# Optimization experiments

Measured on AMD Instinct MI355X. Metric: run time of the kernel, lower is better.

Reference implementation:

```python
import jax, jax.numpy as jnp
import numpy as np

NX, NQ, NU = 2048, 2048, 16
EPS = 0.01
STD = 0.5


def setup_inputs() -> dict:
    key = jax.random.key(0)
    ks = jax.random.split(key, 8)
    return {
        "t": 0,
        "x": jax.random.normal(ks[0], (NX,), dtype=jnp.float32),
        "u": jax.random.normal(ks[1], (NU,), dtype=jnp.float32),
        "X": jax.random.normal(ks[2], (NX + NQ, NX + NQ), dtype=jnp.float32) * STD,
        "U": jax.random.normal(ks[3], (NX, NQ), dtype=jnp.float32) * STD,
        "Y1": jax.random.normal(ks[4], (NX, NX), dtype=jnp.float32) * STD,
        "XP": jax.random.normal(ks[5], (NX, NX), dtype=jnp.float32) * STD,
        "B2": jax.random.normal(ks[6], (NX, NU), dtype=jnp.float32) * STD,
        "D12": jax.random.normal(ks[7], (NQ, NU), dtype=jnp.float32) * STD,
    }


def _constrained_mats(X, U, Y1, XP):
    nx = XP.shape[0]
    nq = U.shape[1]
    # P = XP XP^T + eps I ;  H = X X^T + eps I   (F.linear(A,B)=A@B.T)
    P = XP @ XP.T + EPS * jnp.eye(nx, dtype=XP.dtype)
    H = X @ X.T + EPS * jnp.eye(nx + nq, dtype=X.dtype)
    H11 = H[:nx, :nx]
    H12 = H[:nx, nx:]
    H22 = H[nx:, nx:]
    Y = -0.5 * (H11 + Y1 - Y1.T)
    Pinv = jnp.linalg.inv(P)
    A = Pinv @ Y                        # F.linear(inv(P), Y.T) = inv(P) @ Y
    lam = 0.5 * jnp.diagonal(H22)       # diagonal of Lambda
    D11 = -jnp.tril(H22, -1) / lam[:, None]   # strictly lower triangular
    C1 = U.T / lam[:, None]             # inv(Lambda) @ U.T
    B1 = Pinv @ (-H12 - U)
    return A, B1, C1, D11


def _solve_w(D11, c):
    nq = c.shape[0]

    def step(w, inp):
        i, d_row, ci = inp
        wi = jax.nn.relu(ci + jnp.dot(d_row, w))
        return w.at[i].set(wi), None

    w0 = jnp.zeros(nq, dtype=c.dtype)
    w, _ = jax.lax.scan(step, w0, (jnp.arange(nq), D11, c))
    return w


def reference(t, x, u, X, U, Y1, XP, B2, D12):
    A, B1, C1, D11 = _constrained_mats(X, U, Y1, XP)
    c = C1 @ x + D12 @ u                # precomputed affine part (bv = 0, bias=False)
    w = _solve_w(D11, c)
    x_dot = A @ x + B1 @ w + B2 @ u     # bx = 0
    return x_dot
```

## Files before the change

kernel.cpp:

```cpp
#include <hip/hip_runtime.h>
#include <math.h>

#define NQ2 2048
#define NT  4096
#define NUU 16
#define FEPS 0.01f
#define NB  64
#define NBLK 32
#define NSB 128
#define NSP 132
#define NSBLK 16
#define GCH 16

typedef __attribute__((ext_vector_type(8))) short short8;
typedef __attribute__((ext_vector_type(4))) float floatx4;

__device__ __forceinline__ float readlane_f(float v, int lane) {
  return __int_as_float(__builtin_amdgcn_readlane(__float_as_int(v), lane));
}
__device__ __forceinline__ unsigned short f2bf(float x) {
  unsigned u = __float_as_uint(x);
  unsigned r = u + 0x7FFFu + ((u >> 16) & 1u);
  return (unsigned short)(r >> 16);
}
__device__ __forceinline__ float bf2f(unsigned short h) {
  return __uint_as_float(((unsigned)h) << 16);
}

__device__ __forceinline__ float wave_reduce(float v) {
#pragma unroll
  for (int off = 32; off > 0; off >>= 1) v += __shfl_down(v, off, 64);
  return v;
}
__device__ __forceinline__ float block_reduce_256(float v) {
  __shared__ float sm[4];
  v = wave_reduce(v);
  if ((threadIdx.x & 63) == 0) sm[threadIdx.x >> 6] = v;
  __syncthreads();
  return (threadIdx.x == 0) ? (sm[0] + sm[1] + sm[2] + sm[3]) : 0.0f;
}

__global__ __launch_bounds__(256) void lam_kernel(const float* __restrict__ X,
                                                  float* __restrict__ invlam) {
  int row = blockIdx.x;
  const float* xr = X + (size_t)(NQ2 + row) * NT;
  float s = 0.f;
  for (int k = threadIdx.x * 4; k < NT; k += 1024) {
    float4 v = *(const float4*)(xr + k);
    s += v.x * v.x + v.y * v.y + v.z * v.z + v.w * v.w;
  }
  float tot = block_reduce_256(s);
  if (threadIdx.x == 0) invlam[row] = 1.0f / (0.5f * (tot + FEPS));
}

__global__ __launch_bounds__(256) void tgemv_part_kernel(const float* __restrict__ A,
                                                         const float* __restrict__ v,
                                                         float* __restrict__ part) {
  int col = blockIdx.x * 256 + threadIdx.x;
  int ch = blockIdx.y;
  int i0 = ch * (NQ2 / GCH), i1 = i0 + NQ2 / GCH;
  float s = 0.f;
#pragma unroll 4
  for (int i = i0; i < i1; i++) s = fmaf(A[(size_t)i * NQ2 + col], v[i], s);
  part[(size_t)ch * NQ2 + col] = s;
}

template <int FM>
__global__ __launch_bounds__(256) void finish_kernel(const float* __restrict__ part,
                                                     const float* __restrict__ invlam,
                                                     const float* __restrict__ D12,
                                                     const float* __restrict__ u,
                                                     float* __restrict__ dst) {
  int col = blockIdx.x * 256 + threadIdx.x;
  float s = 0.f;
#pragma unroll
  for (int ch = 0; ch < GCH; ch++) s += part[(size_t)ch * NQ2 + col];
  if (FM == 0) {
    float d = 0.f;
#pragma unroll
    for (int j = 0; j < NUU; j++) d += D12[(size_t)col * NUU + j] * u[j];
    dst[col] = s * invlam[col] + d;
  } else if (FM == 1) {
    dst[col] += 0.5f * s;
  } else {
    dst[col] = s;
  }
}

__device__ void syrk512_body(const float* __restrict__ A, int lda, int K,
                             float* __restrict__ C, float eps, int L, int tid) {
  __shared__ __align__(16) short Ah[4096], Al[4096], Bh[4096], Bl[4096];

  int bi = (int)((sqrtf(8.0f * (float)L + 1.0f) - 1.0f) * 0.5f);
  while ((bi + 1) * (bi + 2) / 2 <= L) bi++;
  while (bi * (bi + 1) / 2 > L) bi--;
  int bj = L - bi * (bi + 1) / 2;
  int row0 = bi * 128, col0 = bj * 128;

  int l = tid & 63;
  int w = tid >> 6;
  int wr = w >> 1, wc = w & 1;

  int g = tid;
  int ar = (g >> 6) * 16 + (g & 15), ak = ((g >> 4) & 3) * 8;
  const float* pa = A + (size_t)(row0 + ar) * lda + ak;
  const float* pb = A + (size_t)(col0 + ar) * lda + ak;

  floatx4 acc[4][4];
#pragma unroll
  for (int m = 0; m < 4; m++)
#pragma unroll
    for (int n = 0; n < 4; n++) acc[m][n] = (floatx4){0.f, 0.f, 0.f, 0.f};

  float xa[8], xb[8];
  {
    float4 t0 = *(const float4*)(pa), t1 = *(const float4*)(pa + 4);
    xa[0]=t0.x; xa[1]=t0.y; xa[2]=t0.z; xa[3]=t0.w; xa[4]=t1.x; xa[5]=t1.y; xa[6]=t1.z; xa[7]=t1.w;
    t0 = *(const float4*)(pb); t1 = *(const float4*)(pb + 4);
    xb[0]=t0.x; xb[1]=t0.y; xb[2]=t0.z; xb[3]=t0.w; xb[4]=t1.x; xb[5]=t1.y; xb[6]=t1.z; xb[7]=t1.w;
  }

  for (int k0 = 0; k0 < K; k0 += 32) {
    __syncthreads();
    {
      short8 h, lo;
#pragma unroll
      for (int j = 0; j < 8; j++) { unsigned short hb = f2bf(xa[j]); h[j] = (short)hb; lo[j] = (short)f2bf(xa[j] - bf2f(hb)); }
      *(short8*)&Ah[g * 8] = h; *(short8*)&Al[g * 8] = lo;
#pragma unroll
      for (int j = 0; j < 8; j++) { unsigned short hb = f2bf(xb[j]); h[j] = (short)hb; lo[j] = (short)f2bf(xb[j] - bf2f(hb)); }
      *(short8*)&Bh[g * 8] = h; *(short8*)&Bl[g * 8] = lo;
    }
    __syncthreads();
    if (k0 + 32 < K) {
      const float* q = pa + k0 + 32;
      float4 t0 = *(const float4*)(q), t1 = *(const float4*)(q + 4);
      xa[0]=t0.x; xa[1]=t0.y; xa[2]=t0.z; xa[3]=t0.w; xa[4]=t1.x; xa[5]=t1.y; xa[6]=t1.z; xa[7]=t1.w;
      q = pb + k0 + 32; t0 = *(const float4*)(q); t1 = *(const float4*)(q + 4);
      xb[0]=t0.x; xb[1]=t0.y; xb[2]=t0.z; xb[3]=t0.w; xb[4]=t1.x; xb[5]=t1.y; xb[6]=t1.z; xb[7]=t1.w;
    }
    if (tid < 256) {
      short8 amh[4], aml[4], bnh[4], bnl[4];
#pragma unroll
      for (int m = 0; m < 4; m++) {
        int ga = ((wr * 4 + m) * 64 + l) * 8;
        amh[m] = *(const short8*)&Ah[ga];
        aml[m] = *(const short8*)&Al[ga];
      }
#pragma unroll
      for (int n = 0; n < 4; n++) {
        int gb = ((wc * 4 + n) * 64 + l) * 8;
        bnh[n] = *(const short8*)&Bh[gb];
        bnl[n] = *(const short8*)&Bl[gb];
      }
#pragma unroll
      for (int m = 0; m < 4; m++)
#pragma unroll
        for (int n = 0; n < 4; n++) {
          acc[m][n] = __builtin_amdgcn_mfma_f32_16x16x32_bf16(amh[m], bnh[n], acc[m][n], 0, 0, 0);
          acc[m][n] = __builtin_amdgcn_mfma_f32_16x16x32_bf16(amh[m], bnl[n], acc[m][n], 0, 0, 0);
          acc[m][n] = __builtin_amdgcn_mfma_f32_16x16x32_bf16(aml[m], bnh[n], acc[m][n], 0, 0, 0);
        }
    }
  }

  if (tid < 256) {
    int lr = (l >> 4) * 4;
    int lc = l & 15;
#pragma unroll
    for (int m = 0; m < 4; m++)
#pragma unroll
      for (int n = 0; n < 4; n++)
#pragma unroll
        for (int r = 0; r < 4; r++) {
          int gi = row0 + wr * 64 + m * 16 + lr + r;
          int gj = col0 + wc * 64 + n * 16 + lc;
          float v = acc[m][n][r];
          if (gi == gj) v += eps;
          C[(size_t)gi * NQ2 + gj] = v;
        }
  }
}

__global__ __launch_bounds__(512) void syrk512_kernel(const float* __restrict__ A,
                                                      int lda, int K,
                                                      float* __restrict__ C, float eps) {
  syrk512_body(A, lda, K, C, eps, blockIdx.x, threadIdx.x);
}

__device__ void wsolve_body(const float* __restrict__ M_, const float* __restrict__ rhs,
                            const float* __restrict__ invlam, float* __restrict__ out,
                            int tid) {
  __shared__ float partial[NQ2];
  __shared__ float il[NQ2];
  __shared__ float tile[2][NB][NB + 1];
  __shared__ float vblk[NB];
  int rquad = tid >> 2;
  int l4 = tid & 3;
  for (int i = tid; i < NQ2; i += 512) {
    partial[i] = rhs[i];
    il[i] = invlam[i];
  }
  for (int e = tid; e < NB * NB; e += 512) {
    int rr = e >> 6, cc = e & 63;
    tile[0][rr][cc] = M_[(size_t)rr * NQ2 + cc];
  }
  __syncthreads();
  for (int b = 0; b < NBLK; b++) {
    int cur = b & 1;
    int b0 = b * NB;
    if (tid < 64) {
      int l = tid;
      float creg = partial[b0 + l];
      float ilreg = il[b0 + l];
      float acc = 0.f;
      float wfin = 0.f;
#pragma unroll
      for (int i = 0; i < NB; i++) {
        float cand = fmaxf(creg - acc * ilreg, 0.f);
        float wi = readlane_f(cand, i);
        acc = fmaf(tile[cur][l][i], wi, acc);
        if (l == i) wfin = wi;
      }
      vblk[l] = wfin;
      out[b0 + l] = wfin;
    } else if (b + 1 < NBLK) {
      int b1 = b0 + NB;
      for (int e = tid - 64; e < NB * NB; e += 448) {
        int rr = e >> 6, cc = e & 63;
        tile[cur ^ 1][rr][cc] = M_[(size_t)(b1 + rr) * NQ2 + b1 + cc];
      }
    }
    __syncthreads();
    float4 v0 = *(const float4*)(&vblk[l4 * 16]);
    float4 v1 = *(const float4*)(&vblk[l4 * 16 + 4]);
    float4 v2 = *(const float4*)(&vblk[l4 * 16 + 8]);
    float4 v3 = *(const float4*)(&vblk[l4 * 16 + 12]);
    for (int base = b0 + NB; base < NQ2; base += 512) {
      float accv[4] = {0.f, 0.f, 0.f, 0.f};
#pragma unroll
      for (int rr = 0; rr < 4; rr++) {
        int row = base + rr * 128 + rquad;
        if (row < NQ2) {
          const float* mr = M_ + (size_t)row * NQ2 + b0 + l4 * 16;
          float4 m0 = *(const float4*)(mr);
          float4 m1 = *(const float4*)(mr + 4);
          float4 m2 = *(const float4*)(mr + 8);
          float4 m3 = *(const float4*)(mr + 12);
          accv[rr] = m0.x * v0.x + m0.y * v0.y + m0.z * v0.z + m0.w * v0.w
                   + m1.x * v1.x + m1.y * v1.y + m1.z * v1.z + m1.w * v1.w
                   + m2.x * v2.x + m2.y * v2.y + m2.z * v2.z + m2.w * v2.w
                   + m3.x * v3.x + m3.y * v3.y + m3.z * v3.z + m3.w * v3.w;
        }
      }
#pragma unroll
      for (int rr = 0; rr < 4; rr++) {
        accv[rr] += __shfl_xor(accv[rr], 1);
        accv[rr] += __shfl_xor(accv[rr], 2);
      }
      if (l4 == 0) {
#pragma unroll
        for (int rr = 0; rr < 4; rr++) {
          int row = base + rr * 128 + rquad;
          if (row < NQ2) partial[row] -= accv[rr] * il[row];
        }
      }
    }
    __syncthreads();
  }
}

__global__ __launch_bounds__(512) void wsolve_kernel(const float* __restrict__ M_,
                                                     const float* __restrict__ rhs,
                                                     const float* __restrict__ invlam,
                                                     float* __restrict__ out) {
  wsolve_body(M_, rhs, invlam, out, threadIdx.x);
}

__global__ __launch_bounds__(512) void merged_wsolve_psyrk_kernel(
    const float* __restrict__ Mh22, const float* __restrict__ c,
    const float* __restrict__ invlam, float* __restrict__ w,
    const float* __restrict__ XP, float* __restrict__ P) {
  if (blockIdx.x == 0) {
    wsolve_body(Mh22, c, invlam, w, threadIdx.x);
  } else {
    syrk512_body(XP, NQ2, NQ2, P, FEPS, blockIdx.x - 1, threadIdx.x);
  }
}

__global__ __launch_bounds__(512) void chol_diag128_kernel(float* __restrict__ M_,
                                                           float* __restrict__ Xinvs, int k) {
  __shared__ __align__(16) float Ls[NSB][NSP];
  __shared__ __align__(16) float Xs[NSB][NSP];
  __shared__ float Tmp[32][33];
  __shared__ float dinv[NSB];
  int b0 = k * NSB;
  int tid = threadIdx.x;
  int wv = tid >> 6;
  int lane = tid & 63;

  for (int e = tid; e < NSB * NSP; e += 512) ((float*)Xs)[e] = 0.f;
  for (int e = tid; e < NSB * NSB; e += 512) {
    int rr = e >> 7, cc = e & 127;
    Ls[rr][cc] = M_[(size_t)(b0 + rr) * NQ2 + b0 + cc];
  }
  __syncthreads();

#pragma unroll 1
  for (int kb = 0; kb < 4; kb++) {
    int o = kb * 32;
    if (wv == 0) {
      int r = lane & 31;
      float a[32];
#pragma unroll
      for (int j = 0; j < 32; j++) a[j] = Ls[o + r][o + j];
#pragma unroll
      for (int j = 0; j < 32; j++) {
        float d = readlane_f(a[j], j);
        float rs = rsqrtf(fmaxf(d, 1e-20f));
        a[j] *= rs;
        if (lane == 0) dinv[o + j] = rs;
#pragma unroll
        for (int k2 = j + 1; k2 < 32; k2++) {
          float ljk = readlane_f(a[j], k2);
          a[k2] = fmaf(-a[j], ljk, a[k2]);
        }
      }
      if (lane < 32) {
#pragma unroll
        for (int j = 0; j < 32; j++) Ls[o + r][o + j] = a[j];
      }
    }
    __syncthreads();
    int nrows = 96 - o;
    if (nrows > 0) {
      if (tid < nrows) {
        int r = o + 32 + tid;
        float v[32];
#pragma unroll
        for (int j = 0; j < 32; j++) v[j] = Ls[r][o + j];
#pragma unroll
        for (int t = 0; t < 32; t++) {
          v[t] *= dinv[o + t];
#pragma unroll
          for (int j = t + 1; j < 32; j++)
            v[j] = fmaf(-v[t], Ls[o + j][o + t], v[j]);
        }
#pragma unroll
        for (int j = 0; j < 32; j++) Ls[r][o + j] = v[j];
      }
      __syncthreads();
      int tot = nrows * (nrows + 1) / 2;
      for (int e = tid; e < tot; e += 512) {
        int a = (int)((sqrtf(8.0f * (float)e + 1.0f) - 1.0f) * 0.5f);
        while ((a + 1) * (a + 2) / 2 <= e) a++;
        while (a * (a + 1) / 2 > e) a--;
        int bcol = e - a * (a + 1) / 2;
        int rr = o + 32 + a, cc = o + 32 + bcol;
        float s = 0.f;
#pragma unroll
        for (int t = 0; t < 32; t += 4) {
          float4 av = *(const float4*)&Ls[rr][o + t];
          float4 bv = *(const float4*)&Ls[cc][o + t];
          s += av.x * bv.x + av.y * bv.y + av.z * bv.z + av.w * bv.w;
        }
        Ls[rr][cc] -= s;
      }
      __syncthreads();
    }
  }

  if (wv < 4) {
    int o = wv * 32;
    int c = lane & 31;
    float x[32];
#pragma unroll
    for (int i = 0; i < 32; i++) x[i] = 0.f;
#pragma unroll
    for (int t = 0; t < 32; t++) {
      float rcpd = 1.0f / Ls[o + t][o + t];
      x[t] = (t == c) ? rcpd : x[t] * rcpd;
#pragma unroll
      for (int i = t + 1; i < 32; i++)
        x[i] = fmaf(-Ls[o + i][o + t], x[t], x[i]);
    }
    if (lane < 32) {
#pragma unroll
      for (int i = 0; i < 32; i++) Xs[o + i][o + c] = x[i];
    }
  }
  __syncthreads();

#pragma unroll 1
  for (int j = 0; j < 4; j++) {
#pragma unroll 1
    for (int i = j + 1; i < 4; i++) {
      int oi = i * 32, oj = j * 32;
      for (int e = tid; e < 32 * 32; e += 512) {
        int rr = e >> 5, cc = e & 31;
        float s = 0.f;
        for (int kk = j; kk < i; kk++) {
          int ok = kk * 32;
#pragma unroll
          for (int t = 0; t < 32; t += 4) {
            float4 a = *(const float4*)&Ls[oi + rr][ok + t];
            s += a.x * Xs[ok + t][oj + cc] + a.y * Xs[ok + t + 1][oj + cc]
               + a.z * Xs[ok + t + 2][oj + cc] + a.w * Xs[ok + t + 3][oj + cc];
          }
        }
        Tmp[rr][cc] = s;
      }
      __syncthreads();
      for (int e = tid; e < 32 * 32; e += 512) {
        int rr = e >> 5, cc = e & 31;
        float s = 0.f;
#pragma unroll
        for (int t = 0; t < 32; t += 4) {
          float4 a = *(const float4*)&Xs[oi + rr][oi + t];
          s += a.x * Tmp[t][cc] + a.y * Tmp[t + 1][cc]
             + a.z * Tmp[t + 2][cc] + a.w * Tmp[t + 3][cc];
        }
        Xs[oi + rr][oj + cc] = -s;
      }
      __syncthreads();
    }
  }

  float* Xp = Xinvs + (size_t)k * NSB * NSB;
  for (int e = tid; e < NSB * NSB; e += 512) {
    int rr = e >> 7, cc = e & 127;
    if (cc <= rr) M_[(size_t)(b0 + rr) * NQ2 + b0 + cc] = Ls[rr][cc];
    Xp[e] = Xs[rr][cc];
  }
}

__device__ void trail512_body(float* __restrict__ M_, int k, int L, int tid) {
  __shared__ float As[16][128];
  __shared__ float Bs[16][128];
  int bi = (int)((sqrtf(8.0f * (float)L + 1.0f) - 1.0f) * 0.5f);
  while ((bi + 1) * (bi + 2) / 2 <= L) bi++;
  while (bi * (bi + 1) / 2 > L) bi--;
  int bj = L - bi * (bi + 1) / 2;
  int row0 = (k + 1 + bi) * NSB, col0 = (k + 1 + bj) * NSB, kc = k * NSB;
  const float* ap = M_ + (size_t)row0 * NQ2 + kc;
  const float* bp = M_ + (size_t)col0 * NQ2 + kc;

  int tx = tid & 15, ty = (tid >> 4) & 15;
  float acc[8][8] = {{0.f}};
  for (int k0 = 0; k0 < 128; k0 += 16) {
    __syncthreads();
    for (int e = tid; e < 1024; e += 512) {
      int isB = e >> 9, idx = e & 511;
      int row = idx >> 2, q = (idx & 3) * 4;
      const float* src = isB ? bp : ap;
      float4 v = *(const float4*)(src + (size_t)row * NQ2 + k0 + q);
      if (isB) { Bs[q][row] = v.x; Bs[q + 1][row] = v.y; Bs[q + 2][row] = v.z; Bs[q + 3][row] = v.w; }
      else     { As[q][row] = v.x; As[q + 1][row] = v.y; As[q + 2][row] = v.z; As[q + 3][row] = v.w; }
    }
    __syncthreads();
    if (tid < 256) {
#pragma unroll
      for (int kk = 0; kk < 16; kk++) {
        float4 aL = *(const float4*)&As[kk][ty * 4];
        float4 aH = *(const float4*)&As[kk][64 + ty * 4];
        float4 bL = *(const float4*)&Bs[kk][tx * 4];
        float4 bH = *(const float4*)&Bs[kk][64 + tx * 4];
        float aa[8] = {aL.x, aL.y, aL.z, aL.w, aH.x, aH.y, aH.z, aH.w};
        float bb[8] = {bL.x, bL.y, bL.z, bL.w, bH.x, bH.y, bH.z, bH.w};
#pragma unroll
        for (int i = 0; i < 8; i++)
#pragma unroll
          for (int j = 0; j < 8; j++) acc[i][j] = fmaf(aa[i], bb[j], acc[i][j]);
      }
    }
  }
  if (tid < 256) {
#pragma unroll
    for (int ii = 0; ii < 8; ii++) {
      int gi = row0 + ((ii >> 2) * 64) + ty * 4 + (ii & 3);
#pragma unroll
      for (int half = 0; half < 2; half++) {
        int gj0 = col0 + half * 64 + tx * 4;
        float* cp = &M_[(size_t)gi * NQ2 + gj0];
        float4 v = *(const float4*)cp;
        v.x -= acc[ii][half * 4 + 0]; v.y -= acc[ii][half * 4 + 1];
        v.z -= acc[ii][half * 4 + 2]; v.w -= acc[ii][half * 4 + 3];
        *(float4*)cp = v;
      }
    }
  }
}

__global__ __launch_bounds__(512) void chol_trail512_kernel(float* __restrict__ M_, int k) {
  trail512_body(M_, k, blockIdx.x, threadIdx.x);
}

__global__ __launch_bounds__(256) void chol_panel128_kernel(float* __restrict__ M_,
                                                            const float* __restrict__ Xinv,
                                                            int k) {
  int kc = k * NSB;
  int rb0 = kc + NSB + blockIdx.x * 128;
  __shared__ float As[16][128];
  __shared__ float Bs[16][128];
  int tid = threadIdx.x;
  int tx = tid & 15, ty = tid >> 4;
  int sr = tid >> 1, ks = (tid & 1) * 8;

  const float* ap = M_ + (size_t)(rb0 + sr) * NQ2 + kc + ks;
  const float* bp = Xinv + sr * 128 + ks;
  float4 a0 = *(const float4*)(ap), a1 = *(const float4*)(ap + 4);
  float4 b0 = *(const float4*)(bp), b1 = *(const float4*)(bp + 4);

  float acc[8][8] = {{0.f}};
  for (int k0 = 0; k0 < 128; k0 += 16) {
    __syncthreads();
    As[ks + 0][sr] = a0.x; As[ks + 1][sr] = a0.y; As[ks + 2][sr] = a0.z; As[ks + 3][sr] = a0.w;
    As[ks + 4][sr] = a1.x; As[ks + 5][sr] = a1.y; As[ks + 6][sr] = a1.z; As[ks + 7][sr] = a1.w;
    Bs[ks + 0][sr] = b0.x; Bs[ks + 1][sr] = b0.y; Bs[ks + 2][sr] = b0.z; Bs[ks + 3][sr] = b0.w;
    Bs[ks + 4][sr] = b1.x; Bs[ks + 5][sr] = b1.y; Bs[ks + 6][sr] = b1.z; Bs[ks + 7][sr] = b1.w;
    __syncthreads();
    if (k0 + 16 < 128) {
      const float* q = ap + k0 + 16;
      a0 = *(const float4*)(q); a1 = *(const float4*)(q + 4);
      q = bp + k0 + 16;
      b0 = *(const float4*)(q); b1 = *(const float4*)(q + 4);
    }
#pragma unroll
    for (int kk = 0; kk < 16; kk++) {
      float4 aL = *(const float4*)&As[kk][ty * 4];
      float4 aH = *(const float4*)&As[kk][64 + ty * 4];
      float4 bL = *(const float4*)&Bs[kk][tx * 4];
      float4 bH = *(const float4*)&Bs[kk][64 + tx * 4];
      float aa[8] = {aL.x, aL.y, aL.z, aL.w, aH.x, aH.y, aH.z, aH.w};
      float bb[8] = {bL.x, bL.y, bL.z, bL.w, bH.x, bH.y, bH.z, bH.w};
#pragma unroll
      for (int i = 0; i < 8; i++)
#pragma unroll
        for (int j = 0; j < 8; j++) acc[i][j] = fmaf(aa[i], bb[j], acc[i][j]);
    }
  }
#pragma unroll
  for (int ii = 0; ii < 8; ii++) {
    int gi = rb0 + ((ii >> 2) * 64) + ty * 4 + (ii & 3);
#pragma unroll
    for (int half = 0; half < 2; half++) {
      int gj0 = kc + half * 64 + tx * 4;
      float4 o;
      o.x = acc[ii][half * 4 + 0]; o.y = acc[ii][half * 4 + 1];
      o.z = acc[ii][half * 4 + 2]; o.w = acc[ii][half * 4 + 3];
      *(float4*)&M_[(size_t)gi * NQ2 + gj0] = o;
    }
  }
}

__global__ __launch_bounds__(1024) void pchsolve_kernel(const float* __restrict__ M_,
                                                        const float* __restrict__ Xinvs,
                                                        const float* __restrict__ rhs,
                                                        float* __restrict__ out) {
  __shared__ float partial[NQ2];
  __shared__ float yv[NQ2];
  __shared__ float Xl[NSB][NSB + 1];
  __shared__ float vblk[NSB];
  int tid = threadIdx.x;
  int row8 = tid >> 3, sub = tid & 7;
  for (int i = tid; i < NQ2; i += 1024) partial[i] = rhs[i];
  __syncthreads();
  for (int kb = 0; kb < NSBLK; kb++) {
    int b0 = kb * NSB;
    const float* Xp = Xinvs + (size_t)kb * NSB * NSB;
    {
      int j0 = sub * 16;
      const float* xr = Xp + row8 * NSB + j0;
      float4 x0 = *(const float4*)(xr), x1 = *(const float4*)(xr + 4);
      float4 x2 = *(const float4*)(xr + 8), x3 = *(const float4*)(xr + 12);
      const float* pp = &partial[b0 + j0];
      float s = x0.x*pp[0] + x0.y*pp[1] + x0.z*pp[2] + x0.w*pp[3]
              + x1.x*pp[4] + x1.y*pp[5] + x1.z*pp[6] + x1.w*pp[7]
              + x2.x*pp[8] + x2.y*pp[9] + x2.z*pp[10] + x2.w*pp[11]
              + x3.x*pp[12] + x3.y*pp[13] + x3.z*pp[14] + x3.w*pp[15];
      s += __shfl_xor(s, 1); s += __shfl_xor(s, 2); s += __shfl_xor(s, 4);
      if (sub == 0) { vblk[row8] = s; yv[b0 + row8] = s; }
    }
    __syncthreads();
    const float* vp = &vblk[sub * 16];
    for (int base = b0 + NSB; base < NQ2; base += 256) {
      int row0 = base + row8;
      int row1 = row0 + 128;
      float s0 = 0.f, s1 = 0.f;
      if (row0 < NQ2) {
        const float* mr = M_ + (size_t)row0 * NQ2 + b0 + sub * 16;
        float4 m0 = *(const float4*)(mr), m1 = *(const float4*)(mr + 4);
        float4 m2 = *(const float4*)(mr + 8), m3 = *(const float4*)(mr + 12);
        s0 = m0.x*vp[0] + m0.y*vp[1] + m0.z*vp[2] + m0.w*vp[3]
           + m1.x*vp[4] + m1.y*vp[5] + m1.z*vp[6] + m1.w*vp[7]
           + m2.x*vp[8] + m2.y*vp[9] + m2.z*vp[10] + m2.w*vp[11]
           + m3.x*vp[12] + m3.y*vp[13] + m3.z*vp[14] + m3.w*vp[15];
      }
      if (row1 < NQ2) {
        const float* mr = M_ + (size_t)row1 * NQ2 + b0 + sub * 16;
        float4 m0 = *(const float4*)(mr), m1 = *(const float4*)(mr + 4);
        float4 m2 = *(const float4*)(mr + 8), m3 = *(const float4*)(mr + 12);
        s1 = m0.x*vp[0] + m0.y*vp[1] + m0.z*vp[2] + m0.w*vp[3]
           + m1.x*vp[4] + m1.y*vp[5] + m1.z*vp[6] + m1.w*vp[7]
           + m2.x*vp[8] + m2.y*vp[9] + m2.z*vp[10] + m2.w*vp[11]
           + m3.x*vp[12] + m3.y*vp[13] + m3.z*vp[14] + m3.w*vp[15];
      }
      s0 += __shfl_xor(s0, 1); s0 += __shfl_xor(s0, 2); s0 += __shfl_xor(s0, 4);
      s1 += __shfl_xor(s1, 1); s1 += __shfl_xor(s1, 2); s1 += __shfl_xor(s1, 4);
      if (sub == 0) {
        if (row0 < NQ2) partial[row0] -= s0;
        if (row1 < NQ2) partial[row1] -= s1;
      }
    }
    __syncthreads();
  }
  for (int i = tid; i < NQ2; i += 1024) partial[i] = yv[i];
  __syncthreads();
  for (int kb = NSBLK - 1; kb >= 0; kb--) {
    int b0 = kb * NSB;
    const float* Xp = Xinvs + (size_t)kb * NSB * NSB;
    for (int e = tid; e < NSB * NSB; e += 1024) Xl[e >> 7][e & 127] = Xp[e];
    __syncthreads();
    {
      int j0 = sub * 16;
      float s = 0.f;
#pragma unroll
      for (int j = 0; j < 16; j++)
        s = fmaf(Xl[j0 + j][row8], partial[b0 + j0 + j], s);
      s += __shfl_xor(s, 1); s += __shfl_xor(s, 2); s += __shfl_xor(s, 4);
      if (sub == 0) { vblk[row8] = s; out[b0 + row8] = s; }
    }
    __syncthreads();
    for (int i = tid; i < b0; i += 1024) {
      float acc = 0.f;
#pragma unroll 16
      for (int j = 0; j < NSB; j++) acc = fmaf(M_[(size_t)(b0 + j) * NQ2 + i], vblk[j], acc);
      partial[i] -= acc;
    }
    __syncthreads();
  }
}

#define TCH 32
__global__ __launch_bounds__(256) void t_partial_kernel(const float* __restrict__ X,
                                                        const float* __restrict__ x,
                                                        const float* __restrict__ w,
                                                        float* __restrict__ tpart) {
  int k4 = (blockIdx.x * 256 + threadIdx.x) * 4;
  int chunk = blockIdx.y;
  int i0 = chunk * (NT / TCH);
  float4 acc = {0.f, 0.f, 0.f, 0.f};
  for (int i = i0; i < i0 + NT / TCH; i++) {
    float cf = (i < NQ2) ? (-0.5f * x[i]) : (-w[i - NQ2]);
    float4 xv = *(const float4*)(X + (size_t)i * NT + k4);
    acc.x += cf * xv.x; acc.y += cf * xv.y; acc.z += cf * xv.z; acc.w += cf * xv.w;
  }
  *(float4*)(tpart + (size_t)chunk * NT + k4) = acc;
}

__global__ __launch_bounds__(256) void t_reduce_kernel(const float* __restrict__ tpart,
                                                       float* __restrict__ t) {
  int k = blockIdx.x * 256 + threadIdx.x;
  float s = 0.f;
#pragma unroll 8
  for (int ch = 0; ch < TCH; ch++) s += tpart[(size_t)ch * NT + k];
  t[k] = s;
}

__global__ __launch_bounds__(256) void r_kernel(const float* __restrict__ X,
                                                const float* __restrict__ Y1,
                                                const float* __restrict__ U,
                                                const float* __restrict__ t,
                                                const float* __restrict__ x,
                                                const float* __restrict__ w,
                                                float* __restrict__ r) {
  int row = blockIdx.x;
  float s1 = 0.f, s2 = 0.f, s3 = 0.f;
  const float* xr = X + (size_t)row * NT;
  for (int k = threadIdx.x * 4; k < NT; k += 1024) {
    float4 a = *(const float4*)(xr + k);
    float4 b = *(const float4*)(t + k);
    s1 += a.x * b.x + a.y * b.y + a.z * b.z + a.w * b.w;
  }
  const float* yr = Y1 + (size_t)row * NQ2;
  const float* ur = U + (size_t)row * NQ2;
  for (int k = threadIdx.x * 4; k < NQ2; k += 1024) {
    float4 a = *(const float4*)(yr + k);
    float4 b = *(const float4*)(x + k);
    s2 += a.x * b.x + a.y * b.y + a.z * b.z + a.w * b.w;
    float4 c2 = *(const float4*)(ur + k);
    float4 d2 = *(const float4*)(w + k);
    s3 += c2.x * d2.x + c2.y * d2.y + c2.z * d2.z + c2.w * d2.w;
  }
  float v = s1 - 0.5f * s2 - s3;
  float tot = block_reduce_256(v);
  if (threadIdx.x == 0) r[row] = tot - 0.5f * FEPS * x[row];
}

__global__ __launch_bounds__(256) void pz2_res_kernel(const float* __restrict__ XP,
                                                      const float* __restrict__ pz1,
                                                      const float* __restrict__ z,
                                                      const float* __restrict__ r,
                                                      float* __restrict__ res) {
  int row = blockIdx.x;
  float s = 0.f;
  const float* xr = XP + (size_t)row * NQ2;
  for (int k = threadIdx.x * 4; k < NQ2; k += 1024) {
    float4 a = *(const float4*)(xr + k);
    float4 b = *(const float4*)(pz1 + k);
    s += a.x * b.x + a.y * b.y + a.z * b.z + a.w * b.w;
  }
  float tot = block_reduce_256(s);
  if (threadIdx.x == 0) res[row] = r[row] - (tot + FEPS * z[row]);
}

__global__ __launch_bounds__(256) void axpy_kernel(float* __restrict__ z,
                                                   const float* __restrict__ dz) {
  int i = blockIdx.x * 256 + threadIdx.x;
  z[i] += dz[i];
}

__global__ __launch_bounds__(256) void out_kernel(const float* __restrict__ z,
                                                  const float* __restrict__ B2,
                                                  const float* __restrict__ u,
                                                  float* __restrict__ out) {
  int i = blockIdx.x * 256 + threadIdx.x;
  float s = 0.f;
#pragma unroll
  for (int j = 0; j < NUU; j++) s += B2[(size_t)i * NUU + j] * u[j];
  out[i] = z[i] + s;
}

extern "C" void kernel_launch(void* const* d_in, const int* in_sizes, int n_in,
                              void* d_out, int out_size, void* d_ws, size_t ws_size,
                              hipStream_t stream) {
  (void)in_sizes; (void)n_in; (void)out_size;
  const float* x   = (const float*)d_in[1];
  const float* u   = (const float*)d_in[2];
  const float* X   = (const float*)d_in[3];
  const float* U   = (const float*)d_in[4];
  const float* Y1  = (const float*)d_in[5];
  const float* XP  = (const float*)d_in[6];
  const float* B2  = (const float*)d_in[7];
  const float* D12 = (const float*)d_in[8];
  float* out = (float*)d_out;

  float* ws     = (float*)d_ws;
  float* M      = ws;
  float* vecs   = ws + (size_t)NQ2 * NQ2;
  float* invlam = vecs;
  float* c      = vecs + 2048;
  float* w      = vecs + 4096;
  float* r      = vecs + 6144;
  float* z      = vecs + 10240;
  float* dz     = vecs + 12288;
  float* res    = vecs + 14336;
  float* t      = vecs + 16384;
  float* tpart  = vecs + 20480;
  float* gpart  = tpart;
  float* Xinvs  = vecs + 20480 + 32 * 4096;
  float* Ptmp   = Xinvs + (size_t)NSBLK * NSB * NSB;

  size_t need_merged = ((size_t)(Ptmp - ws) + (size_t)NQ2 * NQ2) * sizeof(float);
  bool merged = (ws_size >= need_merged);
  float* P = merged ? Ptmp : M;

  int nsyrk = (NQ2 / 128) * (NQ2 / 128 + 1) / 2;
  dim3 gdim(NQ2 / 256, GCH);
  dim3 tg(4, TCH);

  lam_kernel<<<NQ2, 256, 0, stream>>>(X, invlam);
  tgemv_part_kernel<<<gdim, 256, 0, stream>>>(U, x, gpart);
  finish_kernel<0><<<NQ2 / 256, 256, 0, stream>>>(gpart, invlam, D12, u, c);

  syrk512_kernel<<<nsyrk, 512, 0, stream>>>(X + (size_t)NQ2 * NT, NT, NT, M, 0.0f);

  if (merged) {
    merged_wsolve_psyrk_kernel<<<1 + nsyrk, 512, 0, stream>>>(M, c, invlam, w, XP, Ptmp);
  } else {
    wsolve_kernel<<<1, 512, 0, stream>>>(M, c, invlam, w);
  }

  t_partial_kernel<<<tg, 256, 0, stream>>>(X, x, w, tpart);
  t_reduce_kernel<<<NT / 256, 256, 0, stream>>>(tpart, t);
  r_kernel<<<NQ2, 256, 0, stream>>>(X, Y1, U, t, x, w, r);
  tgemv_part_kernel<<<gdim, 256, 0, stream>>>(Y1, x, gpart);
  finish_kernel<1><<<NQ2 / 256, 256, 0, stream>>>(gpart, invlam, D12, u, r);

  if (!merged) {
    syrk512_kernel<<<nsyrk, 512, 0, stream>>>(XP, NQ2, NQ2, P, FEPS);
  }

  for (int k = 0; k < NSBLK; k++) {
    chol_diag128_kernel<<<1, 512, 0, stream>>>(P, Xinvs, k);
    int m = NSBLK - 1 - k;
    if (m > 0) {
      chol_panel128_kernel<<<m, 256, 0, stream>>>(P, Xinvs + (size_t)k * NSB * NSB, k);
      chol_trail512_kernel<<<m * (m + 1) / 2, 512, 0, stream>>>(P, k);
    }
  }

  pchsolve_kernel<<<1, 1024, 0, stream>>>(P, Xinvs, r, z);

  {
    tgemv_part_kernel<<<gdim, 256, 0, stream>>>(XP, z, gpart);
    finish_kernel<2><<<NQ2 / 256, 256, 0, stream>>>(gpart, invlam, D12, u, t);
    pz2_res_kernel<<<NQ2, 256, 0, stream>>>(XP, t, z, r, res);
    pchsolve_kernel<<<1, 1024, 0, stream>>>(P, Xinvs, res, dz);
    axpy_kernel<<<NQ2 / 256, 256, 0, stream>>>(z, dz);
  }

  out_kernel<<<NQ2 / 256, 256, 0, stream>>>(z, B2, u, out);
}
```

Measured before the change: 2.569 ms.

## Co-schedule independent vector work with Cholesky steps via merged multi-role kernels

The H22 SYRK, lambda reduction and U^T x GEMV are fused into one head kernel. The t/r/Y1 GEMV chain is split across the first three Cholesky iterations, with each piece running in the same launch as a diag or trailing-update block. This is meant to fill idle CUs during the serial, low-occupancy Cholesky steps and to cut launch count. In exchange the code becomes more complex and the multi-role kernels have a larger shared-memory and register footprint, which can lower occupancy.

Result: no change. 2.571 ms (+0.1%).

```diff
diff --git a/kernel.cpp b/kernel.cpp
--- a/kernel.cpp
+++ b/kernel.cpp
@@ -53,6 +53,24 @@
   if (threadIdx.x == 0) invlam[row] = 1.0f / (0.5f * (tot + FEPS));
 }
 
+__device__ void lam512_body(const float* __restrict__ X, float* __restrict__ invlam,
+                            int row, int tid) {
+  __shared__ float sm8[8];
+  const float* xr = X + (size_t)(NQ2 + row) * NT;
+  float s = 0.f;
+  for (int k = tid * 4; k < NT; k += 2048) {
+    float4 v = *(const float4*)(xr + k);
+    s += v.x * v.x + v.y * v.y + v.z * v.z + v.w * v.w;
+  }
+  s = wave_reduce(s);
+  if ((tid & 63) == 0) sm8[tid >> 6] = s;
+  __syncthreads();
+  if (tid == 0) {
+    float tot = sm8[0] + sm8[1] + sm8[2] + sm8[3] + sm8[4] + sm8[5] + sm8[6] + sm8[7];
+    invlam[row] = 1.0f / (0.5f * (tot + FEPS));
+  }
+}
+
 __global__ __launch_bounds__(256) void tgemv_part_kernel(const float* __restrict__ A,
                                                          const float* __restrict__ v,
                                                          float* __restrict__ part) {
@@ -65,6 +83,18 @@
   part[(size_t)ch * NQ2 + col] = s;
 }
 
+__device__ void tgemv512_body(const float* __restrict__ A, const float* __restrict__ v,
+                              float* __restrict__ part, int wg, int tid) {
+  int u0 = wg * 512 + tid;
+  int col = u0 & 2047;
+  int ch = u0 >> 11;
+  int i0 = ch * (NQ2 / GCH), i1 = i0 + NQ2 / GCH;
+  float s = 0.f;
+#pragma unroll 4
+  for (int i = i0; i < i1; i++) s = fmaf(A[(size_t)i * NQ2 + col], v[i], s);
+  part[(size_t)ch * NQ2 + col] = s;
+}
+
 template <int FM>
 __global__ __launch_bounds__(256) void finish_kernel(const float* __restrict__ part,
                                                      const float* __restrict__ invlam,
@@ -87,6 +117,15 @@
   }
 }
 
+__device__ void finish1_512_body(const float* __restrict__ part, float* __restrict__ r,
+                                 int wg, int tid) {
+  int col = wg * 512 + tid;
+  float s = 0.f;
+#pragma unroll
+  for (int ch = 0; ch < GCH; ch++) s += part[(size_t)ch * NQ2 + col];
+  r[col] += 0.5f * s;
+}
+
 __device__ void syrk512_body(const float* __restrict__ A, int lda, int K,
                              float* __restrict__ C, float eps, int L, int tid) {
   __shared__ __align__(16) short Ah[4096], Al[4096], Bh[4096], Bl[4096];
@@ -186,6 +225,22 @@
                                                       int lda, int K,
                                                       float* __restrict__ C, float eps) {
   syrk512_body(A, lda, K, C, eps, blockIdx.x, threadIdx.x);
+}
+
+__global__ __launch_bounds__(512) void head_kernel(const float* __restrict__ X,
+                                                   float* __restrict__ M,
+                                                   float* __restrict__ invlam,
+                                                   const float* __restrict__ U,
+                                                   const float* __restrict__ x,
+                                                   float* __restrict__ gpart) {
+  int b = blockIdx.x;
+  if (b < 136) {
+    syrk512_body(X + (size_t)NQ2 * NT, NT, NT, M, 0.0f, b, threadIdx.x);
+  } else if (b < 136 + 2048) {
+    lam512_body(X, invlam, b - 136, threadIdx.x);
+  } else {
+    tgemv512_body(U, x, gpart, b - (136 + 2048), threadIdx.x);
+  }
 }
 
 __device__ void wsolve_body(const float* __restrict__ M_, const float* __restrict__ rhs,
@@ -288,14 +343,13 @@
   }
 }
 
-__global__ __launch_bounds__(512) void chol_diag128_kernel(float* __restrict__ M_,
-                                                           float* __restrict__ Xinvs, int k) {
+__device__ void chol_diag128_body(float* __restrict__ M_, float* __restrict__ Xinvs,
+                                  int k, int tid) {
   __shared__ __align__(16) float Ls[NSB][NSP];
   __shared__ __align__(16) float Xs[NSB][NSP];
   __shared__ float Tmp[32][33];
   __shared__ float dinv[NSB];
   int b0 = k * NSB;
-  int tid = threadIdx.x;
   int wv = tid >> 6;
   int lane = tid & 63;
 
@@ -434,6 +488,11 @@
   }
 }
 
+__global__ __launch_bounds__(512) void chol_diag128_kernel(float* __restrict__ M_,
+                                                           float* __restrict__ Xinvs, int k) {
+  chol_diag128_body(M_, Xinvs, k, threadIdx.x);
+}
+
 __device__ void trail512_body(float* __restrict__ M_, int k, int L, int tid) {
   __shared__ float As[16][128];
   __shared__ float Bs[16][128];
@@ -493,6 +552,111 @@
 
 __global__ __launch_bounds__(512) void chol_trail512_kernel(float* __restrict__ M_, int k) {
   trail512_body(M_, k, blockIdx.x, threadIdx.x);
+}
+
+__device__ void tpart512_body(const float* __restrict__ X, const float* __restrict__ x,
+                              const float* __restrict__ w, float* __restrict__ tpart,
+                              int wg, int tid) {
+  int u0 = wg * 512 + tid;
+  int k4 = (u0 & 1023) * 4;
+  int chunk = u0 >> 10;
+  int i0 = chunk * (NT / 32);
+  float4 acc = {0.f, 0.f, 0.f, 0.f};
+  for (int i = i0; i < i0 + NT / 32; i++) {
+    float cf = (i < NQ2) ? (-0.5f * x[i]) : (-w[i - NQ2]);
+    float4 xv = *(const float4*)(X + (size_t)i * NT + k4);
+    acc.x += cf * xv.x; acc.y += cf * xv.y; acc.z += cf * xv.z; acc.w += cf * xv.w;
+  }
+  *(float4*)(tpart + (size_t)chunk * NT + k4) = acc;
+}
+
+__device__ void treduce512_body(const float* __restrict__ tpart, float* __restrict__ t,
+                                int wg, int tid) {
+  int k = wg * 512 + tid;
+  float s = 0.f;
+#pragma unroll 8
+  for (int ch = 0; ch < 32; ch++) s += tpart[(size_t)ch * NT + k];
+  t[k] = s;
+}
+
+__device__ void rker512_body(const float* __restrict__ X, const float* __restrict__ Y1,
+                             const float* __restrict__ U, const float* __restrict__ t,
+                             const float* __restrict__ x, const float* __restrict__ w,
+                             float* __restrict__ r, int row, int tid) {
+  __shared__ float sm8[8];
+  float s1 = 0.f, s2 = 0.f, s3 = 0.f;
+  const float* xr = X + (size_t)row * NT;
+  for (int k = tid * 4; k < NT; k += 2048) {
+    float4 a = *(const float4*)(xr + k);
+    float4 b = *(const float4*)(t + k);
+    s1 += a.x * b.x + a.y * b.y + a.z * b.z + a.w * b.w;
+  }
+  const float* yr = Y1 + (size_t)row * NQ2;
+  const float* ur = U + (size_t)row * NQ2;
+  for (int k = tid * 4; k < NQ2; k += 2048) {
+    float4 a = *(const float4*)(yr + k);
+    float4 b = *(const float4*)(x + k);
+    s2 += a.x * b.x + a.y * b.y + a.z * b.z + a.w * b.w;
+    float4 c2 = *(const float4*)(ur + k);
+    float4 d2 = *(const float4*)(w + k);
+    s3 += c2.x * d2.x + c2.y * d2.y + c2.z * d2.z + c2.w * d2.w;
+  }
+  float v = s1 - 0.5f * s2 - s3;
+  v = wave_reduce(v);
+  if ((tid & 63) == 0) sm8[tid >> 6] = v;
+  __syncthreads();
+  if (tid == 0) {
+    float tot = sm8[0] + sm8[1] + sm8[2] + sm8[3] + sm8[4] + sm8[5] + sm8[6] + sm8[7];
+    r[row] = tot - 0.5f * FEPS * x[row];
+  }
+}
+
+__global__ __launch_bounds__(512) void diag_tpart_kernel(float* __restrict__ P,
+                                                         float* __restrict__ Xinvs,
+                                                         const float* __restrict__ X,
+                                                         const float* __restrict__ x,
+                                                         const float* __restrict__ w,
+                                                         float* __restrict__ tpart) {
+  if (blockIdx.x == 0) chol_diag128_body(P, Xinvs, 0, threadIdx.x);
+  else tpart512_body(X, x, w, tpart, blockIdx.x - 1, threadIdx.x);
+}
+
+__global__ __launch_bounds__(512) void trail_treduce_kernel(float* __restrict__ P, int k,
+                                                            int ntiles,
+                                                            const float* __restrict__ tpart,
+                                                            float* __restrict__ t) {
+  if (blockIdx.x < ntiles) trail512_body(P, k, blockIdx.x, threadIdx.x);
+  else treduce512_body(tpart, t, blockIdx.x - ntiles, threadIdx.x);
+}
+
+__global__ __launch_bounds__(512) void diag_rker_kernel(float* __restrict__ P,
+                                                        float* __restrict__ Xinvs, int k,
+                                                        const float* __restrict__ X,
+                                                        const float* __restrict__ Y1,
+                                                        const float* __restrict__ U,
+                                                        const float* __restrict__ t,
+                                                        const float* __restrict__ x,
+                                                        const float* __restrict__ w,
+                                                        float* __restrict__ r) {
+  if (blockIdx.x == 0) chol_diag128_body(P, Xinvs, k, threadIdx.x);
+  else rker512_body(X, Y1, U, t, x, w, r, blockIdx.x - 1, threadIdx.x);
+}
+
+__global__ __launch_bounds__(512) void trail_tgemv_kernel(float* __restrict__ P, int k,
+                                                          int ntiles,
+                                                          const float* __restrict__ Y1,
+                                                          const float* __restrict__ x,
+                                                          float* __restrict__ gpart) {
+  if (blockIdx.x < ntiles) trail512_body(P, k, blockIdx.x, threadIdx.x);
+  else tgemv512_body(Y1, x, gpart, blockIdx.x - ntiles, threadIdx.x);
+}
+
+__global__ __launch_bounds__(512) void diag_finish_kernel(float* __restrict__ P,
+                                                          float* __restrict__ Xinvs, int k,
+                                                          const float* __restrict__ gpart,
+                                                          float* __restrict__ r) {
+  if (blockIdx.x == 0) chol_diag128_body(P, Xinvs, k, threadIdx.x);
+  else finish1_512_body(gpart, r, blockIdx.x - 1, threadIdx.x);
 }
 
 __global__ __launch_bounds__(256) void chol_panel128_kernel(float* __restrict__ M_,
@@ -769,34 +933,47 @@
   dim3 gdim(NQ2 / 256, GCH);
   dim3 tg(4, TCH);
 
-  lam_kernel<<<NQ2, 256, 0, stream>>>(X, invlam);
-  tgemv_part_kernel<<<gdim, 256, 0, stream>>>(U, x, gpart);
-  finish_kernel<0><<<NQ2 / 256, 256, 0, stream>>>(gpart, invlam, D12, u, c);
-
-  syrk512_kernel<<<nsyrk, 512, 0, stream>>>(X + (size_t)NQ2 * NT, NT, NT, M, 0.0f);
-
   if (merged) {
+    head_kernel<<<136 + 2048 + 64, 512, 0, stream>>>(X, M, invlam, U, x, gpart);
+    finish_kernel<0><<<NQ2 / 256, 256, 0, stream>>>(gpart, invlam, D12, u, c);
     merged_wsolve_psyrk_kernel<<<1 + nsyrk, 512, 0, stream>>>(M, c, invlam, w, XP, Ptmp);
+
+    diag_tpart_kernel<<<1 + 64, 512, 0, stream>>>(P, Xinvs, X, x, w, tpart);
+    chol_panel128_kernel<<<15, 256, 0, stream>>>(P, Xinvs, 0);
+    trail_treduce_kernel<<<120 + 8, 512, 0, stream>>>(P, 0, 120, tpart, t);
+    diag_rker_kernel<<<1 + 2048, 512, 0, stream>>>(P, Xinvs, 1, X, Y1, U, t, x, w, r);
+    chol_panel128_kernel<<<14, 256, 0, stream>>>(P, Xinvs + (size_t)1 * NSB * NSB, 1);
+    trail_tgemv_kernel<<<105 + 64, 512, 0, stream>>>(P, 1, 105, Y1, x, gpart);
+    diag_finish_kernel<<<1 + 4, 512, 0, stream>>>(P, Xinvs, 2, gpart, r);
+    chol_panel128_kernel<<<13, 256, 0, stream>>>(P, Xinvs + (size_t)2 * NSB * NSB, 2);
+    chol_trail512_kernel<<<91, 512, 0, stream>>>(P, 2);
+    for (int k = 3; k < NSBLK; k++) {
+      chol_diag128_kernel<<<1, 512, 0, stream>>>(P, Xinvs, k);
+      int m = NSBLK - 1 - k;
+      if (m > 0) {
+        chol_panel128_kernel<<<m, 256, 0, stream>>>(P, Xinvs + (size_t)k * NSB * NSB, k);
+        chol_trail512_kernel<<<m * (m + 1) / 2, 512, 0, stream>>>(P, k);
+      }
+    }
   } else {
+    lam_kernel<<<NQ2, 256, 0, stream>>>(X, invlam);
+    tgemv_part_kernel<<<gdim, 256, 0, stream>>>(U, x, gpart);
+    finish_kernel<0><<<NQ2 / 256, 256, 0, stream>>>(gpart, invlam, D12, u, c);
+    syrk512_kernel<<<nsyrk, 512, 0, stream>>>(X + (size_t)NQ2 * NT, NT, NT, M, 0.0f);
     wsolve_kernel<<<1, 512, 0, stream>>>(M, c, invlam, w);
-  }
-
-  t_partial_kernel<<<tg, 256, 0, stream>>>(X, x, w, tpart);
-  t_reduce_kernel<<<NT / 256, 256, 0, stream>>>(tpart, t);
-  r_kernel<<<NQ2, 256, 0, stream>>>(X, Y1, U, t, x, w, r);
-  tgemv_part_kernel<<<gdim, 256, 0, stream>>>(Y1, x, gpart);
-  finish_kernel<1><<<NQ2 / 256, 256, 0, stream>>>(gpart, invlam, D12, u, r);
-
-  if (!merged) {
+    t_partial_kernel<<<tg, 256, 0, stream>>>(X, x, w, tpart);
+    t_reduce_kernel<<<NT / 256, 256, 0, stream>>>(tpart, t);
+    r_kernel<<<NQ2, 256, 0, stream>>>(X, Y1, U, t, x, w, r);
+    tgemv_part_kernel<<<gdim, 256, 0, stream>>>(Y1, x, gpart);
+    finish_kernel<1><<<NQ2 / 256, 256, 0, stream>>>(gpart, invlam, D12, u, r);
     syrk512_kernel<<<nsyrk, 512, 0, stream>>>(XP, NQ2, NQ2, P, FEPS);
-  }
-
-  for (int k = 0; k < NSBLK; k++) {
-    chol_diag128_kernel<<<1, 512, 0, stream>>>(P, Xinvs, k);
-    int m = NSBLK - 1 - k;
-    if (m > 0) {
-      chol_panel128_kernel<<<m, 256, 0, stream>>>(P, Xinvs + (size_t)k * NSB * NSB, k);
-      chol_trail512_kernel<<<m * (m + 1) / 2, 512, 0, stream>>>(P, k);
+    for (int k = 0; k < NSBLK; k++) {
+      chol_diag128_kernel<<<1, 512, 0, stream>>>(P, Xinvs, k);
+      int m = NSBLK - 1 - k;
+      if (m > 0) {
+        chol_panel128_kernel<<<m, 256, 0, stream>>>(P, Xinvs + (size_t)k * NSB * NSB, k);
+        chol_trail512_kernel<<<m * (m + 1) / 2, 512, 0, stream>>>(P, k);
+      }
     }
   }
 
```
